# Performance work log

Hardware: AMD Instinct MI355X
Metric: run time of the kernel (lower is better)

## Reference

```python
import jax, jax.numpy as jnp
import numpy as np

B, N, C, H = 16, 577, 768, 12  # batch, tokens (HW+1), channels, heads
DH = C // H
FF = 4 * C
EPS = 1e-5  # torch LayerNorm default


def layer_norm(x, g, b):
    mu = jnp.mean(x, axis=-1, keepdims=True)
    var = jnp.mean(jnp.square(x - mu), axis=-1, keepdims=True)
    return (x - mu) * jax.lax.rsqrt(var + EPS) * g + b


def setup_inputs() -> dict:
    key = jax.random.key(0)
    ks = jax.random.split(key, 12)
    s = 0.02
    return {
        "x": jax.random.normal(ks[0], (B, N, C), jnp.float32),
        "_EB": 0,
        "ln1_g": jnp.ones((C,), jnp.float32),
        "ln1_b": jnp.zeros((C,), jnp.float32),
        "wq": jax.random.normal(ks[1], (C, C), jnp.float32) * s,
        "bq": jnp.zeros((C,), jnp.float32),
        "wk": jax.random.normal(ks[2], (C, C), jnp.float32) * s,
        "bk": jnp.zeros((C,), jnp.float32),
        "wv": jax.random.normal(ks[3], (C, C), jnp.float32) * s,
        "bv": jnp.zeros((C,), jnp.float32),
        "wo": jax.random.normal(ks[4], (C, C), jnp.float32) * s,
        "bo": jnp.zeros((C,), jnp.float32),
        "ln2_g": jnp.ones((C,), jnp.float32),
        "ln2_b": jnp.zeros((C,), jnp.float32),
        "w1": jax.random.normal(ks[5], (C, FF), jnp.float32) * s,
        "b1": jax.random.normal(ks[6], (FF,), jnp.float32) * 1e-6,
        "w2": jax.random.normal(ks[7], (FF, C), jnp.float32) * s,
        "b2": jax.random.normal(ks[8], (C,), jnp.float32) * 1e-6,
    }


def reference(x, _EB, ln1_g, ln1_b, wq, bq, wk, bk, wv, bv, wo, bo, ln2_g, ln2_b, w1, b1, w2, b2):
    # pre-norm 1 (_EB is falsy -> skipped, as in the original `if _EB:`)
    h = layer_norm(x, ln1_g, ln1_b)
    # MHSA: naive QK^T -> softmax -> V (the original materializes the full matrix)
    q = (h @ wq + bq).reshape(B, N, H, DH).transpose(0, 2, 1, 3)  # (B,H,N,DH)
    k = (h @ wk + bk).reshape(B, N, H, DH).transpose(0, 2, 1, 3)
    v = (h @ wv + bv).reshape(B, N, H, DH).transpose(0, 2, 1, 3)
    sim = jnp.einsum("bhqd,bhkd->bhqk", q, k) / jnp.sqrt(jnp.float32(DH))
    attn = jax.nn.softmax(sim, axis=-1)  # (B,H,N,N)
    o = jnp.einsum("bhqk,bhkd->bhqd", attn, v)
    o = o.transpose(0, 2, 1, 3).reshape(B, N, C) @ wo + bo
    x1 = x + o
    # pre-norm 2 + GELU MLP (torch nn.GELU default = exact erf gelu)
    h2 = layer_norm(x1, ln2_g, ln2_b)
    m = jax.nn.gelu(h2 @ w1 + b1, approximate=False) @ w2 + b2
    return x1 + m
```

## Files before the change

kernel.cpp:

```cpp
#include <hip/hip_runtime.h>
#include <hip/hip_bf16.h>

#define BATCH 16
#define SEQ   577
#define CDIM  768
#define HEADS 12
#define DHEAD 64
#define FFDIM 3072
#define MROWS (BATCH*SEQ)

typedef __bf16 bf16x8 __attribute__((ext_vector_type(8)));
typedef float  f32x4  __attribute__((ext_vector_type(4)));
typedef unsigned short u16x8 __attribute__((ext_vector_type(8)));

__device__ __forceinline__ unsigned short f2bf(float f) {
    unsigned u = __builtin_bit_cast(unsigned, f);
    unsigned r = (u + 0x7FFFu + ((u >> 16) & 1u)) >> 16;
    return (unsigned short)r;
}
__device__ __forceinline__ float bf2f(unsigned short s) {
    return __builtin_bit_cast(float, (unsigned)s << 16);
}
__device__ __forceinline__ float gelu_f(float v) {
    return 0.5f * v * (1.f + erff(v * 0.7071067811865475f));
}
__device__ __forceinline__ void gll16(const void* g, void* l) {
    __builtin_amdgcn_global_load_lds(
        (const __attribute__((address_space(1))) unsigned int*)g,
        (__attribute__((address_space(3))) unsigned int*)l, 16, 0, 0);
}
#define MFMA16(a, b, c) __builtin_amdgcn_mfma_f32_16x16x32_bf16((a), (b), (c), 0, 0, 0)

#define S0 (2304*768)
#define S1 (768*768)
#define S2 (768*3072)
#define S3 (3072*768)
#define STOT (S0+S1+S2+S3)

__global__ __launch_bounds__(256) void convert_w(
    const float* __restrict__ wq, const float* __restrict__ wk, const float* __restrict__ wv,
    const float* __restrict__ wo, const float* __restrict__ w1, const float* __restrict__ w2,
    const float* __restrict__ bq, const float* __restrict__ bk, const float* __restrict__ bv,
    unsigned short* __restrict__ wqkvT, unsigned short* __restrict__ woT,
    unsigned short* __restrict__ w1T, unsigned short* __restrict__ w2T,
    float* __restrict__ bqkv)
{
    for (size_t id = (size_t)blockIdx.x * 256 + threadIdx.x; id < STOT + 2304; id += (size_t)gridDim.x * 256) {
        if (id < S0) {
            int n = (int)(id / 768), k = (int)(id % 768);
            const float* w = (n < 768) ? wq : (n < 1536) ? wk : wv;
            int c = (n < 768) ? n : (n < 1536) ? n - 768 : n - 1536;
            wqkvT[id] = f2bf(w[(size_t)k * 768 + c]);
        } else if (id < S0 + S1) {
            size_t i2 = id - S0; int n = (int)(i2 / 768), k = (int)(i2 % 768);
            woT[i2] = f2bf(wo[(size_t)k * 768 + n]);
        } else if (id < S0 + S1 + S2) {
            size_t i3 = id - S0 - S1; int n = (int)(i3 / 768), k = (int)(i3 % 768);
            w1T[i3] = f2bf(w1[(size_t)k * 3072 + n]);
        } else if (id < STOT) {
            size_t i4 = id - S0 - S1 - S2; int n = (int)(i4 / 3072), k = (int)(i4 % 3072);
            w2T[i4] = f2bf(w2[(size_t)k * 768 + n]);
        } else {
            int c = (int)(id - STOT);
            float v = (c < 768) ? bq[c] : (c < 1536) ? bk[c - 768] : bv[c - 1536];
            bqkv[c] = v;
        }
    }
}

__global__ __launch_bounds__(256) void ln_bf16(
    const float* __restrict__ x, const float* __restrict__ g, const float* __restrict__ b,
    unsigned short* __restrict__ out)
{
    int row = blockIdx.x;
    int t = threadIdx.x;
    const float* xr = x + (size_t)row * CDIM;
    float v0 = xr[t], v1 = xr[t + 256], v2 = xr[t + 512];
    float s = v0 + v1 + v2;
    float q = v0 * v0 + v1 * v1 + v2 * v2;
    __shared__ float red[8];
    for (int o = 32; o > 0; o >>= 1) { s += __shfl_down(s, o); q += __shfl_down(q, o); }
    int wid = t >> 6;
    if ((t & 63) == 0) { red[wid] = s; red[4 + wid] = q; }
    __syncthreads();
    if (t == 0) {
        float S = red[0] + red[1] + red[2] + red[3];
        float Q = red[4] + red[5] + red[6] + red[7];
        float mu = S * (1.f / CDIM);
        float var = Q * (1.f / CDIM) - mu * mu;
        red[0] = mu; red[1] = rsqrtf(var + 1e-5f);
    }
    __syncthreads();
    float mu = red[0], rs = red[1];
    unsigned short* orow = out + (size_t)row * CDIM;
    orow[t]       = f2bf((v0 - mu) * rs * g[t]       + b[t]);
    orow[t + 256] = f2bf((v1 - mu) * rs * g[t + 256] + b[t + 256]);
    orow[t + 512] = f2bf((v2 - mu) * rs * g[t + 512] + b[t + 512]);
}

template<int EPI>
__global__ __launch_bounds__(512, 4) void gemm128(
    const unsigned short* __restrict__ A, const unsigned short* __restrict__ Bt,
    const float* __restrict__ bias, void* __restrict__ Cout,
    const float* __restrict__ resid, int M, int Nn, int K)
{
    __shared__ __align__(16) unsigned short As[2][128][32];
    __shared__ __align__(16) unsigned short Bs[2][128][32];

    int t = threadIdx.x;
    int gx = gridDim.x;
    int nwg = gx * gridDim.y;
    int bid = blockIdx.y * gx + blockIdx.x;
    int qc = nwg >> 3, rc = nwg & 7;
    int xcd = bid & 7, loc = bid >> 3;
    int swz = (xcd < rc ? xcd * (qc + 1) : rc * (qc + 1) + (xcd - rc) * qc) + loc;
    int nbase = (swz % gx) * 128;
    int mbase = (swz / gx) * 128;

    int lane = t & 63, w = t >> 6;
    int wm = w >> 2, wn = w & 3;
    int lr = lane & 15, lk = lane >> 4;
    int k0 = lk * 8;

    int srow = lane >> 2;
    int scol = (lane & 3) * 8;

    int arow = min(mbase + w * 16 + srow, M - 1);
    int brow = nbase + w * 16 + srow;
    const unsigned short* ap = A  + (size_t)arow * K + scol;
    const unsigned short* bp = Bt + (size_t)brow * K + scol;
    char* lA[2] = { (char*)&As[0][0][0] + w * 1024, (char*)&As[1][0][0] + w * 1024 };
    char* lB[2] = { (char*)&Bs[0][0][0] + w * 1024, (char*)&Bs[1][0][0] + w * 1024 };

    f32x4 acc[4][2] = {};

    gll16(ap, lA[0]);
    gll16(bp, lB[0]);

    for (int kt = 0; kt < K; kt += 32) {
        int buf = (kt >> 5) & 1;
        __syncthreads();
        if (kt + 32 < K) {
            gll16(ap + kt + 32, lA[buf ^ 1]);
            gll16(bp + kt + 32, lB[buf ^ 1]);
        }
        bf16x8 af[4], bfv[2];
#pragma unroll
        for (int mi = 0; mi < 4; mi++) af[mi]  = *(const bf16x8*)&As[buf][wm * 64 + mi * 16 + lr][k0];
#pragma unroll
        for (int ni = 0; ni < 2; ni++) bfv[ni] = *(const bf16x8*)&Bs[buf][wn * 32 + ni * 16 + lr][k0];
#pragma unroll
        for (int mi = 0; mi < 4; mi++)
#pragma unroll
            for (int ni = 0; ni < 2; ni++)
                acc[mi][ni] = MFMA16(af[mi], bfv[ni], acc[mi][ni]);
    }

#pragma unroll
    for (int mi = 0; mi < 4; mi++) {
#pragma unroll
        for (int ni = 0; ni < 2; ni++) {
            int col = nbase + wn * 32 + ni * 16 + lr;
            float bcol = bias[col];
#pragma unroll
            for (int i = 0; i < 4; i++) {
                int row = mbase + wm * 64 + mi * 16 + lk * 4 + i;
                if (row >= M) continue;
                float v = acc[mi][ni][i] + bcol;
                if (EPI == 0) {
                    ((unsigned short*)Cout)[(size_t)row * Nn + col] = f2bf(v);
                } else if (EPI == 1) {
                    ((float*)Cout)[(size_t)row * Nn + col] = resid[(size_t)row * Nn + col] + v;
                } else {
                    ((unsigned short*)Cout)[(size_t)row * Nn + col] = f2bf(gelu_f(v));
                }
            }
        }
    }
}

__global__ __launch_bounds__(256) void attn_kernel(
    const unsigned short* __restrict__ qkv, unsigned short* __restrict__ attno)
{
    int bh = blockIdx.y;
    int b = bh / HEADS, h = bh % HEADS;
    int qt = blockIdx.x;
    int t = threadIdx.x;
    int lane = t & 63, w = t >> 6;
    int lr = lane & 15, lk = lane >> 4, k0 = lk * 8;

    const size_t baseRow = (size_t)b * SEQ;
    const unsigned short* Qp = qkv + baseRow * 2304 + h * 64;
    const unsigned short* Kp = Qp + 768;
    const unsigned short* Vp = Qp + 1536;

    __shared__ __align__(16) unsigned short sSP[32][648];
    __shared__ __align__(16) unsigned short sVt[64 * 64];
    __shared__ float sRedM[4][32];
    __shared__ float sRedS[4][32];

    bf16x8 afr[2][2];
#pragma unroll
    for (int mi = 0; mi < 2; mi++) {
        int qr = qt * 32 + mi * 16 + lr; if (qr > SEQ - 1) qr = SEQ - 1;
#pragma unroll
        for (int ks = 0; ks < 2; ks++)
            afr[mi][ks] = *(const bf16x8*)(Qp + (size_t)qr * 2304 + ks * 32 + k0);
    }
    int jp = t >> 3;
    int dg = (t & 7) * 8;
    u16x8 vA, vB;
    vA = *(const u16x8*)(Vp + (size_t)min(jp * 2,     SEQ - 1) * 2304 + dg);
    vB = *(const u16x8*)(Vp + (size_t)min(jp * 2 + 1, SEQ - 1) * 2304 + dg);

    f32x4 acc[10][2];
    float mx[2][4];
#pragma unroll
    for (int mi = 0; mi < 2; mi++)
#pragma unroll
        for (int i = 0; i < 4; i++) mx[mi][i] = -1e30f;

#pragma unroll
    for (int it = 0; it < 10; it++) {
        int jt = w + it * 4;
        int col = jt * 16 + lr;
        int j = min(col, SEQ - 1);
        f32x4 a0 = {}, a1 = {};
#pragma unroll
        for (int ks = 0; ks < 2; ks++) {
            bf16x8 bfr = *(const bf16x8*)(Kp + (size_t)j * 2304 + ks * 32 + k0);
            a0 = MFMA16(afr[0][ks], bfr, a0);
            a1 = MFMA16(afr[1][ks], bfr, a1);
        }
        acc[it][0] = a0; acc[it][1] = a1;
        if (col < SEQ) {
#pragma unroll
            for (int i = 0; i < 4; i++) {
                mx[0][i] = fmaxf(mx[0][i], a0[i]);
                mx[1][i] = fmaxf(mx[1][i], a1[i]);
            }
        }
    }
#pragma unroll
    for (int mi = 0; mi < 2; mi++) {
#pragma unroll
        for (int i = 0; i < 4; i++) {
            float v = mx[mi][i];
            v = fmaxf(v, __shfl_xor(v, 1));
            v = fmaxf(v, __shfl_xor(v, 2));
            v = fmaxf(v, __shfl_xor(v, 4));
            v = fmaxf(v, __shfl_xor(v, 8));
            mx[mi][i] = v;
        }
    }
    if (lr == 0)
#pragma unroll
        for (int mi = 0; mi < 2; mi++)
#pragma unroll
            for (int i = 0; i < 4; i++)
                sRedM[w][mi * 16 + lk * 4 + i] = mx[mi][i];
    __syncthreads();

    float rm[2][4], sm[2][4];
#pragma unroll
    for (int mi = 0; mi < 2; mi++)
#pragma unroll
        for (int i = 0; i < 4; i++) {
            int ri = mi * 16 + lk * 4 + i;
            rm[mi][i] = fmaxf(fmaxf(sRedM[0][ri], sRedM[1][ri]),
                              fmaxf(sRedM[2][ri], sRedM[3][ri]));
            sm[mi][i] = 0.f;
        }
#pragma unroll
    for (int it = 0; it < 10; it++) {
        int jt = w + it * 4;
        int col = jt * 16 + lr;
        bool valid = col < SEQ;
#pragma unroll
        for (int mi = 0; mi < 2; mi++) {
#pragma unroll
            for (int i = 0; i < 4; i++) {
                float p = valid ? __expf(0.125f * (acc[it][mi][i] - rm[mi][i])) : 0.f;
                sm[mi][i] += p;
                sSP[mi * 16 + lk * 4 + i][col] = f2bf(p);
            }
        }
    }
#pragma unroll
    for (int mi = 0; mi < 2; mi++) {
#pragma unroll
        for (int i = 0; i < 4; i++) {
            float v = sm[mi][i];
            v += __shfl_xor(v, 1);
            v += __shfl_xor(v, 2);
            v += __shfl_xor(v, 4);
            v += __shfl_xor(v, 8);
            sm[mi][i] = v;
        }
    }
    if (lr == 0)
#pragma unroll
        for (int mi = 0; mi < 2; mi++)
#pragma unroll
            for (int i = 0; i < 4; i++)
                sRedS[w][mi * 16 + lk * 4 + i] = sm[mi][i];
    __syncthreads();

    f32x4 oacc[2] = {};
    int d = w * 16 + lr;
    int fx = ((d & 7) ^ (d >> 3)) << 4;
    for (int jc = 0; jc < 10; jc++) {
        __syncthreads();
#pragma unroll
        for (int e = 0; e < 8; e++) {
            unsigned val = (unsigned)vA[e] | ((unsigned)vB[e] << 16);
            int r = dg + e;
            int off = (r * 128 + jp * 4) ^ ((((r & 7) ^ (r >> 3)) & 7) << 4);
            *(unsigned*)((char*)sVt + off) = val;
        }
        if (jc < 9) {
            int j0 = (jc + 1) * 64 + jp * 2;
            vA = *(const u16x8*)(Vp + (size_t)min(j0,     SEQ - 1) * 2304 + dg);
            vB = *(const u16x8*)(Vp + (size_t)min(j0 + 1, SEQ - 1) * 2304 + dg);
        }
        __syncthreads();
#pragma unroll
        for (int ks = 0; ks < 2; ks++) {
            bf16x8 vb = *(const bf16x8*)((char*)sVt + ((d * 128 + ks * 64 + lk * 16) ^ fx));
#pragma unroll
            for (int mi = 0; mi < 2; mi++) {
                bf16x8 pa = *(const bf16x8*)&sSP[mi * 16 + lr][jc * 64 + ks * 32 + k0];
                oacc[mi] = MFMA16(pa, vb, oacc[mi]);
            }
        }
    }

#pragma unroll
    for (int mi = 0; mi < 2; mi++) {
#pragma unroll
        for (int i = 0; i < 4; i++) {
            int ri = mi * 16 + lk * 4 + i;
            int qr = qt * 32 + ri;
            if (qr < SEQ) {
                float rs = sRedS[0][ri] + sRedS[1][ri] + sRedS[2][ri] + sRedS[3][ri];
                float ov = oacc[mi][i] / rs;
                attno[(baseRow + qr) * CDIM + h * 64 + w * 16 + lr] = f2bf(ov);
            }
        }
    }
}

extern "C" void kernel_launch(void* const* d_in, const int* in_sizes, int n_in,
                              void* d_out, int out_size, void* d_ws, size_t ws_size,
                              hipStream_t stream) {
    const float* x     = (const float*)d_in[0];
    const float* ln1_g = (const float*)d_in[2];
    const float* ln1_b = (const float*)d_in[3];
    const float* wq    = (const float*)d_in[4];
    const float* bq    = (const float*)d_in[5];
    const float* wk    = (const float*)d_in[6];
    const float* bk    = (const float*)d_in[7];
    const float* wv    = (const float*)d_in[8];
    const float* bv    = (const float*)d_in[9];
    const float* wo    = (const float*)d_in[10];
    const float* bo    = (const float*)d_in[11];
    const float* ln2_g = (const float*)d_in[12];
    const float* ln2_b = (const float*)d_in[13];
    const float* w1    = (const float*)d_in[14];
    const float* b1    = (const float*)d_in[15];
    const float* w2    = (const float*)d_in[16];
    const float* b2    = (const float*)d_in[17];
    float* out = (float*)d_out;

    char* ws = (char*)d_ws;
    unsigned short* wqkvT = (unsigned short*)(ws + 0);
    unsigned short* woT   = (unsigned short*)(ws + 3538944);
    unsigned short* w1T   = (unsigned short*)(ws + 4718592);
    unsigned short* w2T   = (unsigned short*)(ws + 9437184);
    float*          bqkv  = (float*)         (ws + 14155776);
    unsigned short* qkv   = (unsigned short*)(ws + 14164992);
    unsigned short* hbuf  = (unsigned short*)(ws + 56706048);
    unsigned short* attno = (unsigned short*)(ws + 70886400);
    unsigned short* mid   = (unsigned short*)(ws + 14164992);
    unsigned short* h2    = attno;

    convert_w<<<4096, 256, 0, stream>>>(wq, wk, wv, wo, w1, w2, bq, bk, bv,
                                        wqkvT, woT, w1T, w2T, bqkv);
    ln_bf16<<<MROWS, 256, 0, stream>>>(x, ln1_g, ln1_b, hbuf);
    gemm128<0><<<dim3(2304 / 128, (MROWS + 127) / 128), 512, 0, stream>>>(
        hbuf, wqkvT, bqkv, qkv, nullptr, MROWS, 2304, 768);
    attn_kernel<<<dim3(19, BATCH * HEADS), 256, 0, stream>>>(qkv, attno);
    gemm128<1><<<dim3(768 / 128, (MROWS + 127) / 128), 512, 0, stream>>>(
        attno, woT, bo, out, x, MROWS, 768, 768);
    ln_bf16<<<MROWS, 256, 0, stream>>>(out, ln2_g, ln2_b, h2);
    gemm128<2><<<dim3(3072 / 128, (MROWS + 127) / 128), 512, 0, stream>>>(
        h2, w1T, b1, mid, nullptr, MROWS, 3072, 768);
    gemm128<1><<<dim3(768 / 128, (MROWS + 127) / 128), 512, 0, stream>>>(
        mid, w2T, b2, out, out, MROWS, 768, 3072);
}
```

Before: 374.6 us.

## Use three-stage LDS pipeline with explicit vmcnt waits in GEMM

Changes the GEMM main loop from double buffering to a three-stage shared-memory ring, keeping two global-to-LDS tile loads in flight. Each iteration waits with s_waitcnt vmcnt(2) and a raw barrier instead of __syncthreads, so it only waits for the current stage to land. The goal is to hide global load latency behind MFMA work. The cost is 50% more LDS per block, which may lower occupancy under launch_bounds(512,4), and hand-written waitcnt assumptions that depend on the load instruction count.

```diff
diff --git a/kernel.cpp b/kernel.cpp
--- a/kernel.cpp
+++ b/kernel.cpp
@@ -104,8 +104,8 @@
     const float* __restrict__ bias, void* __restrict__ Cout,
     const float* __restrict__ resid, int M, int Nn, int K)
 {
-    __shared__ __align__(16) unsigned short As[2][128][32];
-    __shared__ __align__(16) unsigned short Bs[2][128][32];
+    __shared__ __align__(16) unsigned short As[3][128][32];
+    __shared__ __align__(16) unsigned short Bs[3][128][32];
 
     int t = threadIdx.x;
     int gx = gridDim.x;
@@ -129,32 +129,45 @@
     int brow = nbase + w * 16 + srow;
     const unsigned short* ap = A  + (size_t)arow * K + scol;
     const unsigned short* bp = Bt + (size_t)brow * K + scol;
-    char* lA[2] = { (char*)&As[0][0][0] + w * 1024, (char*)&As[1][0][0] + w * 1024 };
-    char* lB[2] = { (char*)&Bs[0][0][0] + w * 1024, (char*)&Bs[1][0][0] + w * 1024 };
+
+    const int nt = K >> 5;
+
+#define STAGE(tk, s)                                                   \
+    {                                                                  \
+        gll16(ap + (tk) * 32, (char*)&As[s][0][0] + w * 1024);         \
+        gll16(bp + (tk) * 32, (char*)&Bs[s][0][0] + w * 1024);         \
+    }
 
     f32x4 acc[4][2] = {};
 
-    gll16(ap, lA[0]);
-    gll16(bp, lB[0]);
-
-    for (int kt = 0; kt < K; kt += 32) {
-        int buf = (kt >> 5) & 1;
-        __syncthreads();
-        if (kt + 32 < K) {
-            gll16(ap + kt + 32, lA[buf ^ 1]);
-            gll16(bp + kt + 32, lB[buf ^ 1]);
-        }
+    STAGE(0, 0);
+    STAGE(1, 1);
+
+    int sc = 0;
+    int sp2 = 2;
+    for (int tk = 0; tk < nt; ++tk) {
+        if (tk + 1 < nt) { asm volatile("s_waitcnt vmcnt(2)" ::: "memory"); }
+        else             { asm volatile("s_waitcnt vmcnt(0)" ::: "memory"); }
+        __builtin_amdgcn_s_barrier();
+        asm volatile("" ::: "memory");
+
+        if (tk + 2 < nt) STAGE(tk + 2, sp2);
+
         bf16x8 af[4], bfv[2];
 #pragma unroll
-        for (int mi = 0; mi < 4; mi++) af[mi]  = *(const bf16x8*)&As[buf][wm * 64 + mi * 16 + lr][k0];
-#pragma unroll
-        for (int ni = 0; ni < 2; ni++) bfv[ni] = *(const bf16x8*)&Bs[buf][wn * 32 + ni * 16 + lr][k0];
+        for (int mi = 0; mi < 4; mi++) af[mi]  = *(const bf16x8*)&As[sc][wm * 64 + mi * 16 + lr][k0];
+#pragma unroll
+        for (int ni = 0; ni < 2; ni++) bfv[ni] = *(const bf16x8*)&Bs[sc][wn * 32 + ni * 16 + lr][k0];
 #pragma unroll
         for (int mi = 0; mi < 4; mi++)
 #pragma unroll
             for (int ni = 0; ni < 2; ni++)
                 acc[mi][ni] = MFMA16(af[mi], bfv[ni], acc[mi][ni]);
-    }
+
+        sc  = (sc  == 2) ? 0 : sc  + 1;
+        sp2 = (sp2 == 2) ? 0 : sp2 + 1;
+    }
+#undef STAGE
 
 #pragma unroll
     for (int mi = 0; mi < 4; mi++) {
```

Measured after the change: 377.3 us. No clear change (+0.7%).

## Deepen GEMM K-tile to 64 with XOR-swizzled LDS layout

Applied to the files above, without the earlier changes.

Doubles the GEMM K step from 32 to 64, so each thread issues two global-to-LDS loads per operand per stage and the loop runs half as many barriers. The LDS tiles are stored with an XOR swizzle on the 16-byte column chunk, keyed by row, which is meant to avoid bank conflicts on the 128-byte rows. LDS use doubles to 64 KB per block, which may limit how many blocks fit on a CU under the 4-blocks launch bound.

```diff
diff --git a/kernel.cpp b/kernel.cpp
--- a/kernel.cpp
+++ b/kernel.cpp
@@ -104,8 +104,8 @@
     const float* __restrict__ bias, void* __restrict__ Cout,
     const float* __restrict__ resid, int M, int Nn, int K)
 {
-    __shared__ __align__(16) unsigned short As[2][128][32];
-    __shared__ __align__(16) unsigned short Bs[2][128][32];
+    __shared__ __align__(16) unsigned short As[2][128 * 64];
+    __shared__ __align__(16) unsigned short Bs[2][128 * 64];
 
     int t = threadIdx.x;
     int gx = gridDim.x;
@@ -120,40 +120,61 @@
     int lane = t & 63, w = t >> 6;
     int wm = w >> 2, wn = w & 3;
     int lr = lane & 15, lk = lane >> 4;
-    int k0 = lk * 8;
-
-    int srow = lane >> 2;
-    int scol = (lane & 3) * 8;
-
-    int arow = min(mbase + w * 16 + srow, M - 1);
-    int brow = nbase + w * 16 + srow;
-    const unsigned short* ap = A  + (size_t)arow * K + scol;
-    const unsigned short* bp = Bt + (size_t)brow * K + scol;
-    char* lA[2] = { (char*)&As[0][0][0] + w * 1024, (char*)&As[1][0][0] + w * 1024 };
-    char* lB[2] = { (char*)&Bs[0][0][0] + w * 1024, (char*)&Bs[1][0][0] + w * 1024 };
+
+    int srow = lane >> 3;
+    int scol = ((lane & 7) * 8) ^ (srow << 3);
+
+    int arow0 = min(mbase + w * 16 + srow,     M - 1);
+    int arow1 = min(mbase + w * 16 + 8 + srow, M - 1);
+    int brow0 = nbase + w * 16 + srow;
+    int brow1 = nbase + w * 16 + 8 + srow;
+    const unsigned short* ap0 = A  + (size_t)arow0 * K + scol;
+    const unsigned short* ap1 = A  + (size_t)arow1 * K + scol;
+    const unsigned short* bp0 = Bt + (size_t)brow0 * K + scol;
+    const unsigned short* bp1 = Bt + (size_t)brow1 * K + scol;
+    char* lA[2] = { (char*)&As[0][0] + w * 2048, (char*)&As[1][0] + w * 2048 };
+    char* lB[2] = { (char*)&Bs[0][0] + w * 2048, (char*)&Bs[1][0] + w * 2048 };
 
     f32x4 acc[4][2] = {};
 
-    gll16(ap, lA[0]);
-    gll16(bp, lB[0]);
-
-    for (int kt = 0; kt < K; kt += 32) {
-        int buf = (kt >> 5) & 1;
+    gll16(ap0, lA[0]);
+    gll16(ap1, lA[0] + 1024);
+    gll16(bp0, lB[0]);
+    gll16(bp1, lB[0] + 1024);
+
+    for (int kt = 0; kt < K; kt += 64) {
+        int buf = (kt >> 6) & 1;
         __syncthreads();
-        if (kt + 32 < K) {
-            gll16(ap + kt + 32, lA[buf ^ 1]);
-            gll16(bp + kt + 32, lB[buf ^ 1]);
-        }
-        bf16x8 af[4], bfv[2];
-#pragma unroll
-        for (int mi = 0; mi < 4; mi++) af[mi]  = *(const bf16x8*)&As[buf][wm * 64 + mi * 16 + lr][k0];
-#pragma unroll
-        for (int ni = 0; ni < 2; ni++) bfv[ni] = *(const bf16x8*)&Bs[buf][wn * 32 + ni * 16 + lr][k0];
-#pragma unroll
-        for (int mi = 0; mi < 4; mi++)
-#pragma unroll
-            for (int ni = 0; ni < 2; ni++)
-                acc[mi][ni] = MFMA16(af[mi], bfv[ni], acc[mi][ni]);
+        if (kt + 64 < K) {
+            gll16(ap0 + kt + 64, lA[buf ^ 1]);
+            gll16(ap1 + kt + 64, lA[buf ^ 1] + 1024);
+            gll16(bp0 + kt + 64, lB[buf ^ 1]);
+            gll16(bp1 + kt + 64, lB[buf ^ 1] + 1024);
+        }
+        bf16x8 af[4][2], bfv[2][2];
+#pragma unroll
+        for (int mi = 0; mi < 4; mi++) {
+            int row = wm * 64 + mi * 16 + lr;
+#pragma unroll
+            for (int ks = 0; ks < 2; ks++)
+                af[mi][ks] = *(const bf16x8*)((char*)&As[buf][0] + row * 128 +
+                                (((ks * 64 + lk * 16)) ^ ((lr & 7) << 4)));
+        }
+#pragma unroll
+        for (int ni = 0; ni < 2; ni++) {
+            int row = wn * 32 + ni * 16 + lr;
+#pragma unroll
+            for (int ks = 0; ks < 2; ks++)
+                bfv[ni][ks] = *(const bf16x8*)((char*)&Bs[buf][0] + row * 128 +
+                                (((ks * 64 + lk * 16)) ^ ((lr & 7) << 4)));
+        }
+#pragma unroll
+        for (int ks = 0; ks < 2; ks++)
+#pragma unroll
+            for (int mi = 0; mi < 4; mi++)
+#pragma unroll
+                for (int ni = 0; ni < 2; ni++)
+                    acc[mi][ni] = MFMA16(af[mi][ks], bfv[ni][ks], acc[mi][ni]);
     }
 
 #pragma unroll
```

New measurement: 358.4 us. 4.3% less time.
